# Performance work log

Measured on AMD Instinct MI355X. Metric: run time of the kernel, lower is better.

Reference implementation:

```python
import jax, jax.numpy as jnp
import numpy as np

N, E = 20000, 320000
IN, H, C = 1024, 8, 64
HC = H * C
EDGE_DIM = 16
NUM_GRAPHS = 8
LEAKY_SLOPE = 0.2
LN_EPS = 1e-5


def setup_inputs() -> dict:
    key = jax.random.key(0)
    ks = jax.random.split(key, 12)
    s = 0.05
    return {
        "x": jax.random.normal(ks[0], (N, IN), jnp.float32),
        "edge_attr": jax.random.normal(ks[1], (E, EDGE_DIM), jnp.float32),
        "edge_index": jax.random.randint(ks[2], (2, E), 0, N, dtype=jnp.int64),
        "batch": jnp.sort(jax.random.randint(ks[3], (N,), 0, NUM_GRAPHS, dtype=jnp.int64)),
        "W_src": jax.random.normal(ks[4], (IN, HC), jnp.float32) * s,
        "W_dst": jax.random.normal(ks[5], (IN, HC), jnp.float32) * s,
        "att_src": jax.random.normal(ks[6], (H, C), jnp.float32) * s,
        "att_dst": jax.random.normal(ks[7], (H, C), jnp.float32) * s,
        "bias": jnp.zeros((HC,), jnp.float32),
        "ln_gamma": jnp.ones((HC,), jnp.float32),
        "ln_beta": jnp.zeros((HC,), jnp.float32),
        "prelu_a": jnp.full((HC,), 0.25, jnp.float32),
    }


def reference(x, edge_attr, edge_index, batch, W_src, W_dst, att_src, att_dst,
              bias, ln_gamma, ln_beta, prelu_a):
    # Eval mode: node/edge feature dropout and attention dropout are identity.
    # with_edge == 'N': edge_attr is unused by the conv.
    n = x.shape[0]
    src, dst = edge_index[0], edge_index[1]

    xs = (x @ W_src).reshape(n, H, C)   # source-side projections
    xd = (x @ W_dst).reshape(n, H, C)   # dest-side projections
    a_src = jnp.einsum('nhc,hc->nh', xs, att_src)
    a_dst = jnp.einsum('nhc,hc->nh', xd, att_dst)

    # edge scores + softmax over incoming edges of each destination node
    e = jax.nn.leaky_relu(a_src[src] + a_dst[dst], LEAKY_SLOPE)  # [E,H]
    m = jax.ops.segment_max(e, dst, num_segments=n)              # [N,H]
    m = jax.lax.stop_gradient(jnp.where(jnp.isfinite(m), m, 0.0))
    ex = jnp.exp(e - m[dst])
    denom = jax.ops.segment_sum(ex, dst, num_segments=n)
    alpha = ex / (denom[dst] + 1e-16)                            # [E,H]

    msg = alpha[:, :, None] * xs[src]                            # [E,H,C]
    out = jax.ops.segment_sum(msg, dst, num_segments=n).reshape(n, HC) + bias

    # norm_type == 'layer': the per-graph boolean-mask loop applies LayerNorm
    # row-wise; with sorted batch ids this equals a single LayerNorm over all
    # nodes (LayerNorm has no cross-row statistics).
    mu = jnp.mean(out, axis=-1, keepdims=True)
    var = jnp.mean(jnp.square(out - mu), axis=-1, keepdims=True)
    y = (out - mu) * jax.lax.rsqrt(var + LN_EPS) * ln_gamma + ln_beta

    # PReLU with per-channel slope
    return jnp.where(y >= 0, y, prelu_a * y)
```

## Files before the change

### kernel.cpp

```cpp
#include <hip/hip_runtime.h>
#include <hip/hip_bf16.h>

#define N_NODES 20000
#define N_EDGES 320000
#define IN_DIM  1024
#define H_HEADS 8
#define C_CH    64
#define HC      512
#define LEAKY   0.2f
#define LN_EPS  1e-5f

#define BCOLS 576

typedef short bf16x8 __attribute__((ext_vector_type(8)));
typedef float f32x4  __attribute__((ext_vector_type(4)));

__device__ __forceinline__ unsigned short f2bf(float f) {
    union { float f; unsigned int u; } c; c.f = f;
    unsigned int u = c.u;
    unsigned int r = (u + 0x7fffu + ((u >> 16) & 1u)) >> 16;
    return (unsigned short)r;
}
__device__ __forceinline__ float bf2f(unsigned int h) {
    union { unsigned int u; float f; } c; c.u = h << 16; return c.f;
}
__device__ __forceinline__ void gload_lds16(const void* g, void* l) {
    __builtin_amdgcn_global_load_lds(
        (const __attribute__((address_space(1))) unsigned int*)g,
        (__attribute__((address_space(3))) unsigned int*)l, 16, 0, 0);
}

#define DEG_BLOCKS 1250
#define CONV_BLOCKS 2048

__global__ __launch_bounds__(256) void fused_pre(
        const float* __restrict__ x, short* __restrict__ xb,
        const int* __restrict__ ei, int* __restrict__ deg) {
    int t = threadIdx.x;
    if (blockIdx.x < DEG_BLOCKS) {
        int e = blockIdx.x * 256 + t;
        atomicAdd(&deg[ei[N_EDGES + e]], 1);
        return;
    }
    int bid = blockIdx.x - DEG_BLOCKS;
    const int total = N_NODES * IN_DIM / 8;
    int stride = CONV_BLOCKS * 256;
    for (int i = bid * 256 + t; i < total; i += stride) {
        float4 a = ((const float4*)x)[(size_t)i * 2];
        float4 b = ((const float4*)x)[(size_t)i * 2 + 1];
        uint4 r;
        r.x = (unsigned int)f2bf(a.x) | ((unsigned int)f2bf(a.y) << 16);
        r.y = (unsigned int)f2bf(a.z) | ((unsigned int)f2bf(a.w) << 16);
        r.z = (unsigned int)f2bf(b.x) | ((unsigned int)f2bf(b.y) << 16);
        r.w = (unsigned int)f2bf(b.z) | ((unsigned int)f2bf(b.w) << 16);
        *(uint4*)(&xb[(size_t)i * 8]) = r;
    }
}

__global__ void prep_w_scan(const float* __restrict__ Wsrc,
                            const float* __restrict__ Wdst,
                            const float* __restrict__ att_src,
                            const float* __restrict__ att_dst,
                            short* __restrict__ wbT,
                            const int* __restrict__ deg,
                            int* __restrict__ off,
                            int* __restrict__ cursor) {
    int t = threadIdx.x;

    if (blockIdx.x == IN_DIM) {
        __shared__ int wtot[2];
        int lane = t & 63, w = t >> 6;
        const int4* deg4 = (const int4*)deg;
        int s = 0;
        if (t < 125) {
            #pragma unroll
            for (int j = 0; j < 40; ++j) {
                int4 u = deg4[t * 40 + j];
                s += u.x + u.y + u.z + u.w;
            }
        }
        int v = s;
        #pragma unroll
        for (int o = 1; o < 64; o <<= 1) {
            int u = __shfl_up(v, o);
            if (lane >= o) v += u;
        }
        if (lane == 63) wtot[w] = v;
        __syncthreads();
        int add = (w == 1) ? wtot[0] : 0;
        int run = add + v - s;
        if (t < 125) {
            int4* off4 = (int4*)off;
            int4* cur4 = (int4*)cursor;
            #pragma unroll
            for (int j = 0; j < 40; ++j) {
                int4 u = deg4[t * 40 + j];
                int4 o_;
                o_.x = run;
                o_.y = o_.x + u.x;
                o_.z = o_.y + u.y;
                o_.w = o_.z + u.z;
                off4[t * 40 + j] = o_;
                cur4[t * 40 + j] = o_;
                run = o_.w + u.w;
            }
            if (t == 124) off[N_NODES] = run;
        }
        return;
    }

    int k = blockIdx.x;
    float4 v = *(const float4*)(Wsrc + (size_t)k * HC + t * 4);
    wbT[(size_t)(t * 4 + 0) * IN_DIM + k] = (short)f2bf(v.x);
    wbT[(size_t)(t * 4 + 1) * IN_DIM + k] = (short)f2bf(v.y);
    wbT[(size_t)(t * 4 + 2) * IN_DIM + k] = (short)f2bf(v.z);
    wbT[(size_t)(t * 4 + 3) * IN_DIM + k] = (short)f2bf(v.w);
    if (t < 16) {
        int h = t & 7;
        const float* W   = (t < 8) ? Wsrc : Wdst;
        const float* att = (t < 8) ? att_src : att_dst;
        float s = 0.f;
        #pragma unroll
        for (int c = 0; c < C_CH; ++c)
            s += W[(size_t)k * HC + h * C_CH + c] * att[h * C_CH + c];
        wbT[(size_t)(512 + t) * IN_DIM + k] = (short)f2bf(s);
    } else if (t < 64) {
        wbT[(size_t)(512 + t) * IN_DIM + k] = 0;
    }
}

#define BM 64
#define BN 96
#define BK 64
#define NCOLT (BCOLS / BN)
#define NROWT ((N_NODES + BM - 1) / BM)
#define NWG (NCOLT * NROWT)
#define KSTEPS (IN_DIM / BK)
#define A_SLOTS (BM * BK / 8)
#define B_SLOTS (BN * BK / 8)

__global__ __launch_bounds__(256) void gemm_scatter(
        const short* __restrict__ xb,
        const short* __restrict__ wbT,
        short* __restrict__ xsb,
        float* __restrict__ a_srcv,
        float* __restrict__ a_dstv,
        const int* __restrict__ ei,
        int* __restrict__ cursor,
        int* __restrict__ csr_src) {
    __shared__ short As[A_SLOTS * 8];
    __shared__ short Bs[B_SLOTS * 8];

    int t = threadIdx.x;

    if (blockIdx.x >= NWG) {
        int e = (blockIdx.x - NWG) * 256 + t;
        int d = ei[N_EDGES + e];
        int idx = atomicAdd(&cursor[d], 1);
        csr_src[idx] = ei[e];
        return;
    }

    int orig = blockIdx.x;
    const int q = NWG >> 3, r = NWG & 7;
    int xcd  = orig & 7;
    int wgid = (xcd < r ? xcd * (q + 1) : r * (q + 1) + (xcd - r) * q) + (orig >> 3);
    int col0 = (wgid % NCOLT) * BN;
    int row0 = (wgid / NCOLT) * BM;

    int lane = t & 63;
    int w    = t >> 6;
    int lr   = lane & 15;
    int lg   = lane >> 4;
    int sw   = lr & 7;
    int wr   = (w >> 1) * 32;
    int wc   = (w & 1) * 48;

    const short* a_base[2];
    #pragma unroll
    for (int i = 0; i < 2; ++i) {
        int s  = t + 256 * i;
        int m  = s >> 3;
        int kc = (s & 7) ^ (m & 7);
        int gm = row0 + m;
        if (gm >= N_NODES) gm = N_NODES - 1;
        a_base[i] = xb + (size_t)gm * IN_DIM + kc * 8;
    }
    const short* b_base[3];
    #pragma unroll
    for (int i = 0; i < 3; ++i) {
        int s  = t + 256 * i;
        int c  = s >> 3;
        int kc = (s & 7) ^ (c & 7);
        b_base[i] = wbT + (size_t)(col0 + c) * IN_DIM + kc * 8;
    }

    f32x4 acc[2][3] = {};

    for (int step = 0; step < KSTEPS; ++step) {
        int k0 = step * BK;
        #pragma unroll
        for (int i = 0; i < 2; ++i)
            gload_lds16(a_base[i] + k0, &As[(t + 256 * i) * 8]);
        #pragma unroll
        for (int i = 0; i < 3; ++i)
            gload_lds16(b_base[i] + k0, &Bs[(t + 256 * i) * 8]);
        asm volatile("s_waitcnt vmcnt(0)" ::: "memory");
        __builtin_amdgcn_s_barrier();

        #pragma unroll
        for (int ks = 0; ks < 2; ++ks) {
            int kc  = ks * 4 + lg;
            int kca = kc ^ sw;
            bf16x8 af[2], bfr[3];
            #pragma unroll
            for (int mi = 0; mi < 2; ++mi)
                af[mi] = *(const bf16x8*)(&As[((wr + mi * 16 + lr) * 8 + kca) * 8]);
            #pragma unroll
            for (int ni = 0; ni < 3; ++ni)
                bfr[ni] = *(const bf16x8*)(&Bs[((wc + ni * 16 + lr) * 8 + kca) * 8]);
            __builtin_amdgcn_s_setprio(1);
            #pragma unroll
            for (int mi = 0; mi < 2; ++mi)
                #pragma unroll
                for (int ni = 0; ni < 3; ++ni)
                    acc[mi][ni] = __builtin_amdgcn_mfma_f32_16x16x32_bf16(
                        af[mi], bfr[ni], acc[mi][ni], 0, 0, 0);
            __builtin_amdgcn_s_setprio(0);
        }
        __builtin_amdgcn_s_barrier();
    }

    #pragma unroll
    for (int mi = 0; mi < 2; ++mi) {
        #pragma unroll
        for (int rr = 0; rr < 4; ++rr) {
            int row = row0 + wr + mi * 16 + lg * 4 + rr;
            if (row >= N_NODES) continue;
            #pragma unroll
            for (int ni = 0; ni < 3; ++ni) {
                int col = col0 + wc + ni * 16 + lr;
                float v = acc[mi][ni][rr];
                if (col < 512)      xsb[(size_t)row * HC + col] = (short)f2bf(v);
                else if (col < 520) a_srcv[(size_t)row * 8 + (col - 512)] = v;
                else if (col < 528) a_dstv[(size_t)row * 8 + (col - 520)] = v;
            }
        }
    }
}

__global__ __launch_bounds__(256) void aggregate_ln(
        const int* __restrict__ off,
        const int* __restrict__ csr_src,
        const float* __restrict__ a_srcv,
        const float* __restrict__ a_dstv,
        const short* __restrict__ xsb,
        const float* __restrict__ bias,
        const float* __restrict__ gamma,
        const float* __restrict__ beta,
        const float* __restrict__ prelu_a,
        float* __restrict__ out) {
    int lane = threadIdx.x & 63;
    int n    = blockIdx.x * 4 + (threadIdx.x >> 6);
    int ch0  = lane * 8;
    int h    = lane >> 3;

    int start = off[n], end = off[n + 1];
    float ad  = a_dstv[(size_t)n * 8 + h];

    float acc[8] = {};
    float wsum = 0.f;

    int i = start;
    for (; i + 1 < end; i += 2) {
        int s0 = __builtin_amdgcn_readfirstlane(csr_src[i]);
        int s1 = __builtin_amdgcn_readfirstlane(csr_src[i + 1]);
        float sc0 = a_srcv[(size_t)s0 * 8 + h] + ad;
        float sc1 = a_srcv[(size_t)s1 * 8 + h] + ad;
        uint4 u0 = *(const uint4*)(xsb + (size_t)s0 * HC + ch0);
        uint4 u1 = *(const uint4*)(xsb + (size_t)s1 * HC + ch0);
        sc0 = (sc0 >= 0.f) ? sc0 : LEAKY * sc0;
        sc1 = (sc1 >= 0.f) ? sc1 : LEAKY * sc1;
        float w0 = __expf(sc0);
        float w1 = __expf(sc1);
        acc[0] = fmaf(w0, bf2f(u0.x & 0xffffu), acc[0]);
        acc[1] = fmaf(w0, bf2f(u0.x >> 16),     acc[1]);
        acc[2] = fmaf(w0, bf2f(u0.y & 0xffffu), acc[2]);
        acc[3] = fmaf(w0, bf2f(u0.y >> 16),     acc[3]);
        acc[4] = fmaf(w0, bf2f(u0.z & 0xffffu), acc[4]);
        acc[5] = fmaf(w0, bf2f(u0.z >> 16),     acc[5]);
        acc[6] = fmaf(w0, bf2f(u0.w & 0xffffu), acc[6]);
        acc[7] = fmaf(w0, bf2f(u0.w >> 16),     acc[7]);
        acc[0] = fmaf(w1, bf2f(u1.x & 0xffffu), acc[0]);
        acc[1] = fmaf(w1, bf2f(u1.x >> 16),     acc[1]);
        acc[2] = fmaf(w1, bf2f(u1.y & 0xffffu), acc[2]);
        acc[3] = fmaf(w1, bf2f(u1.y >> 16),     acc[3]);
        acc[4] = fmaf(w1, bf2f(u1.z & 0xffffu), acc[4]);
        acc[5] = fmaf(w1, bf2f(u1.z >> 16),     acc[5]);
        acc[6] = fmaf(w1, bf2f(u1.w & 0xffffu), acc[6]);
        acc[7] = fmaf(w1, bf2f(u1.w >> 16),     acc[7]);
        wsum += w0 + w1;
    }
    if (i < end) {
        int s0 = __builtin_amdgcn_readfirstlane(csr_src[i]);
        float sc0 = a_srcv[(size_t)s0 * 8 + h] + ad;
        uint4 u0 = *(const uint4*)(xsb + (size_t)s0 * HC + ch0);
        sc0 = (sc0 >= 0.f) ? sc0 : LEAKY * sc0;
        float w0 = __expf(sc0);
        acc[0] = fmaf(w0, bf2f(u0.x & 0xffffu), acc[0]);
        acc[1] = fmaf(w0, bf2f(u0.x >> 16),     acc[1]);
        acc[2] = fmaf(w0, bf2f(u0.y & 0xffffu), acc[2]);
        acc[3] = fmaf(w0, bf2f(u0.y >> 16),     acc[3]);
        acc[4] = fmaf(w0, bf2f(u0.z & 0xffffu), acc[4]);
        acc[5] = fmaf(w0, bf2f(u0.z >> 16),     acc[5]);
        acc[6] = fmaf(w0, bf2f(u0.w & 0xffffu), acc[6]);
        acc[7] = fmaf(w0, bf2f(u0.w >> 16),     acc[7]);
        wsum += w0;
    }

    float inv = 1.f / (wsum + 1e-16f);
    float4 b0 = *(const float4*)(bias + ch0);
    float4 b1 = *(const float4*)(bias + ch0 + 4);
    float v8[8];
    float psum = 0.f, psq = 0.f;
    const float bb[8] = {b0.x, b0.y, b0.z, b0.w, b1.x, b1.y, b1.z, b1.w};
    #pragma unroll
    for (int j = 0; j < 8; ++j) {
        v8[j] = acc[j] * inv + bb[j];
        psum += v8[j];
        psq  += v8[j] * v8[j];
    }
    #pragma unroll
    for (int o = 32; o > 0; o >>= 1) {
        psum += __shfl_xor(psum, o);
        psq  += __shfl_xor(psq, o);
    }
    float mu   = psum * (1.f / (float)HC);
    float var  = psq * (1.f / (float)HC) - mu * mu;
    float rstd = rsqrtf(var + LN_EPS);

    float4 g0 = *(const float4*)(gamma + ch0);
    float4 g1 = *(const float4*)(gamma + ch0 + 4);
    float4 e0 = *(const float4*)(beta + ch0);
    float4 e1 = *(const float4*)(beta + ch0 + 4);
    float4 p0 = *(const float4*)(prelu_a + ch0);
    float4 p1 = *(const float4*)(prelu_a + ch0 + 4);
    const float gg[8] = {g0.x, g0.y, g0.z, g0.w, g1.x, g1.y, g1.z, g1.w};
    const float ee[8] = {e0.x, e0.y, e0.z, e0.w, e1.x, e1.y, e1.z, e1.w};
    const float pp[8] = {p0.x, p0.y, p0.z, p0.w, p1.x, p1.y, p1.z, p1.w};
    float y[8];
    #pragma unroll
    for (int j = 0; j < 8; ++j) {
        float v = (v8[j] - mu) * rstd * gg[j] + ee[j];
        y[j] = (v >= 0.f) ? v : pp[j] * v;
    }
    float4* o4 = (float4*)(out + (size_t)n * HC + ch0);
    o4[0] = make_float4(y[0], y[1], y[2], y[3]);
    o4[1] = make_float4(y[4], y[5], y[6], y[7]);
}

extern "C" void kernel_launch(void* const* d_in, const int* in_sizes, int n_in,
                              void* d_out, int out_size, void* d_ws, size_t ws_size,
                              hipStream_t stream) {
    const float* x        = (const float*)d_in[0];
    const int*   ei       = (const int*)d_in[2];
    const float* Wsrc     = (const float*)d_in[4];
    const float* Wdst     = (const float*)d_in[5];
    const float* att_src  = (const float*)d_in[6];
    const float* att_dst  = (const float*)d_in[7];
    const float* bias     = (const float*)d_in[8];
    const float* gamma    = (const float*)d_in[9];
    const float* beta     = (const float*)d_in[10];
    const float* prelu_a  = (const float*)d_in[11];
    float* out            = (float*)d_out;

    char*  ws = (char*)d_ws;
    size_t o  = 0;
    auto alloc = [&](size_t bytes) -> void* {
        void* p = ws + o;
        o += (bytes + 255) & ~(size_t)255;
        return p;
    };
    short* wbT     = (short*)alloc(sizeof(short) * BCOLS * IN_DIM);
    short* xsb     = (short*)alloc(sizeof(short) * (size_t)N_NODES * HC);
    float* a_srcv  = (float*)alloc(sizeof(float) * N_NODES * 8);
    float* a_dstv  = (float*)alloc(sizeof(float) * N_NODES * 8);
    int*   deg     = (int*)alloc(sizeof(int) * N_NODES);
    int*   off     = (int*)alloc(sizeof(int) * (N_NODES + 1));
    int*   cursor  = (int*)alloc(sizeof(int) * N_NODES);
    int*   csr_src = (int*)alloc(sizeof(int) * N_EDGES);

    short* xb = (short*)d_out;

    hipMemsetAsync(deg, 0, sizeof(int) * N_NODES, stream);

    fused_pre<<<DEG_BLOCKS + CONV_BLOCKS, 256, 0, stream>>>(x, xb, ei, deg);

    prep_w_scan<<<IN_DIM + 1, 128, 0, stream>>>(Wsrc, Wdst, att_src, att_dst,
                                                wbT, deg, off, cursor);

    gemm_scatter<<<NWG + DEG_BLOCKS, 256, 0, stream>>>(
        xb, wbT, xsb, a_srcv, a_dstv, ei, cursor, csr_src);

    aggregate_ln<<<N_NODES / 4, 256, 0, stream>>>(
        off, csr_src, a_srcv, a_dstv, xsb, bias, gamma, beta, prelu_a, out);
}
```

Baseline: 154.7 us.

## Fuse fp32-to-bf16 conversion of x into GEMM A-tile loading

Removes the separate pass that converted x to a bf16 scratch buffer. The GEMM now reads fp32 x directly, converts it in registers, and stores the bf16 A tile to LDS, while B still uses async global-to-LDS loads. This saves a full write and re-read of the bf16 copy. In exchange, each x row is read as fp32 by all six column tiles instead of as bf16, and A loads become synchronous register round-trips without prefetch overlap.

```diff
diff --git a/kernel.cpp b/kernel.cpp
--- a/kernel.cpp
+++ b/kernel.cpp
@@ -24,6 +24,9 @@
 __device__ __forceinline__ float bf2f(unsigned int h) {
     union { unsigned int u; float f; } c; c.u = h << 16; return c.f;
 }
+__device__ __forceinline__ unsigned int bfpack(float lo, float hi) {
+    return (unsigned int)f2bf(lo) | ((unsigned int)f2bf(hi) << 16);
+}
 __device__ __forceinline__ void gload_lds16(const void* g, void* l) {
     __builtin_amdgcn_global_load_lds(
         (const __attribute__((address_space(1))) unsigned int*)g,
@@ -31,30 +34,11 @@
 }
 
 #define DEG_BLOCKS 1250
-#define CONV_BLOCKS 2048
-
-__global__ __launch_bounds__(256) void fused_pre(
-        const float* __restrict__ x, short* __restrict__ xb,
+
+__global__ __launch_bounds__(256) void deg_hist(
         const int* __restrict__ ei, int* __restrict__ deg) {
-    int t = threadIdx.x;
-    if (blockIdx.x < DEG_BLOCKS) {
-        int e = blockIdx.x * 256 + t;
-        atomicAdd(&deg[ei[N_EDGES + e]], 1);
-        return;
-    }
-    int bid = blockIdx.x - DEG_BLOCKS;
-    const int total = N_NODES * IN_DIM / 8;
-    int stride = CONV_BLOCKS * 256;
-    for (int i = bid * 256 + t; i < total; i += stride) {
-        float4 a = ((const float4*)x)[(size_t)i * 2];
-        float4 b = ((const float4*)x)[(size_t)i * 2 + 1];
-        uint4 r;
-        r.x = (unsigned int)f2bf(a.x) | ((unsigned int)f2bf(a.y) << 16);
-        r.y = (unsigned int)f2bf(a.z) | ((unsigned int)f2bf(a.w) << 16);
-        r.z = (unsigned int)f2bf(b.x) | ((unsigned int)f2bf(b.y) << 16);
-        r.w = (unsigned int)f2bf(b.z) | ((unsigned int)f2bf(b.w) << 16);
-        *(uint4*)(&xb[(size_t)i * 8]) = r;
-    }
+    int e = blockIdx.x * 256 + threadIdx.x;
+    atomicAdd(&deg[ei[N_EDGES + e]], 1);
 }
 
 __global__ void prep_w_scan(const float* __restrict__ Wsrc,
@@ -140,7 +124,7 @@
 #define B_SLOTS (BN * BK / 8)
 
 __global__ __launch_bounds__(256) void gemm_scatter(
-        const short* __restrict__ xb,
+        const float* __restrict__ x,
         const short* __restrict__ wbT,
         short* __restrict__ xsb,
         float* __restrict__ a_srcv,
@@ -176,7 +160,7 @@
     int wr   = (w >> 1) * 32;
     int wc   = (w & 1) * 48;
 
-    const short* a_base[2];
+    const float* a_base[2];
     #pragma unroll
     for (int i = 0; i < 2; ++i) {
         int s  = t + 256 * i;
@@ -184,7 +168,7 @@
         int kc = (s & 7) ^ (m & 7);
         int gm = row0 + m;
         if (gm >= N_NODES) gm = N_NODES - 1;
-        a_base[i] = xb + (size_t)gm * IN_DIM + kc * 8;
+        a_base[i] = x + (size_t)gm * IN_DIM + kc * 8;
     }
     const short* b_base[3];
     #pragma unroll
@@ -200,13 +184,20 @@
     for (int step = 0; step < KSTEPS; ++step) {
         int k0 = step * BK;
         #pragma unroll
-        for (int i = 0; i < 2; ++i)
-            gload_lds16(a_base[i] + k0, &As[(t + 256 * i) * 8]);
+        for (int i = 0; i < 2; ++i) {
+            float4 fa = *(const float4*)(a_base[i] + k0);
+            float4 fb = *(const float4*)(a_base[i] + k0 + 4);
+            uint4 rr;
+            rr.x = bfpack(fa.x, fa.y);
+            rr.y = bfpack(fa.z, fa.w);
+            rr.z = bfpack(fb.x, fb.y);
+            rr.w = bfpack(fb.z, fb.w);
+            *(uint4*)(&As[(t + 256 * i) * 8]) = rr;
+        }
         #pragma unroll
         for (int i = 0; i < 3; ++i)
             gload_lds16(b_base[i] + k0, &Bs[(t + 256 * i) * 8]);
-        asm volatile("s_waitcnt vmcnt(0)" ::: "memory");
-        __builtin_amdgcn_s_barrier();
+        __syncthreads();
 
         #pragma unroll
         for (int ks = 0; ks < 2; ++ks) {
@@ -228,7 +219,7 @@
                         af[mi], bfr[ni], acc[mi][ni], 0, 0, 0);
             __builtin_amdgcn_s_setprio(0);
         }
-        __builtin_amdgcn_s_barrier();
+        __syncthreads();
     }
 
     #pragma unroll
@@ -390,17 +381,15 @@
     int*   cursor  = (int*)alloc(sizeof(int) * N_NODES);
     int*   csr_src = (int*)alloc(sizeof(int) * N_EDGES);
 
-    short* xb = (short*)d_out;
-
     hipMemsetAsync(deg, 0, sizeof(int) * N_NODES, stream);
 
-    fused_pre<<<DEG_BLOCKS + CONV_BLOCKS, 256, 0, stream>>>(x, xb, ei, deg);
+    deg_hist<<<DEG_BLOCKS, 256, 0, stream>>>(ei, deg);
 
     prep_w_scan<<<IN_DIM + 1, 128, 0, stream>>>(Wsrc, Wdst, att_src, att_dst,
                                                 wbT, deg, off, cursor);
 
     gemm_scatter<<<NWG + DEG_BLOCKS, 256, 0, stream>>>(
-        xb, wbT, xsb, a_srcv, a_dstv, ei, cursor, csr_src);
+        x, wbT, xsb, a_srcv, a_dstv, ei, cursor, csr_src);
 
     aggregate_ln<<<N_NODES / 4, 256, 0, stream>>>(
         off, csr_src, a_srcv, a_dstv, xsb, bias, gamma, beta, prelu_a, out);
```

Result: faster. 148.0 us (-4.4%).

## Regroup pre-pass kernels and unroll edge aggregation loop by four

Applied to the files above, without the earlier changes.

The degree histogram becomes its own kernel, and the x-to-bf16 conversion is fused with the weight transpose and prefix scan into one mid-pass kernel. The weight prep now overlaps with the large conversion instead of running in a separate launch. The aggregation loop is unrolled to four edges per iteration through a macro, so more gathers can be in flight per wave. In exchange, the weight-prep and scan blocks run at 256 threads with half of them idle, and the unroll adds register pressure.

```diff
diff --git a/kernel.cpp b/kernel.cpp
--- a/kernel.cpp
+++ b/kernel.cpp
@@ -31,101 +31,103 @@
 }
 
 #define DEG_BLOCKS 1250
+
+__global__ __launch_bounds__(256) void deg_hist(
+        const int* __restrict__ ei, int* __restrict__ deg) {
+    int e = blockIdx.x * 256 + threadIdx.x;
+    atomicAdd(&deg[ei[N_EDGES + e]], 1);
+}
+
 #define CONV_BLOCKS 2048
-
-__global__ __launch_bounds__(256) void fused_pre(
+#define PREP_BLOCKS 1024
+
+__global__ __launch_bounds__(256) void mid_pass(
         const float* __restrict__ x, short* __restrict__ xb,
-        const int* __restrict__ ei, int* __restrict__ deg) {
-    int t = threadIdx.x;
-    if (blockIdx.x < DEG_BLOCKS) {
-        int e = blockIdx.x * 256 + t;
-        atomicAdd(&deg[ei[N_EDGES + e]], 1);
+        const float* __restrict__ Wsrc, const float* __restrict__ Wdst,
+        const float* __restrict__ att_src, const float* __restrict__ att_dst,
+        short* __restrict__ wbT,
+        const int* __restrict__ deg, int* __restrict__ off,
+        int* __restrict__ cursor) {
+    int t   = threadIdx.x;
+    int bid = blockIdx.x;
+
+    if (bid < CONV_BLOCKS) {
+        const int total = N_NODES * IN_DIM / 8;
+        int stride = CONV_BLOCKS * 256;
+        for (int i = bid * 256 + t; i < total; i += stride) {
+            float4 a = ((const float4*)x)[(size_t)i * 2];
+            float4 b = ((const float4*)x)[(size_t)i * 2 + 1];
+            uint4 r;
+            r.x = (unsigned int)f2bf(a.x) | ((unsigned int)f2bf(a.y) << 16);
+            r.y = (unsigned int)f2bf(a.z) | ((unsigned int)f2bf(a.w) << 16);
+            r.z = (unsigned int)f2bf(b.x) | ((unsigned int)f2bf(b.y) << 16);
+            r.w = (unsigned int)f2bf(b.z) | ((unsigned int)f2bf(b.w) << 16);
+            *(uint4*)(&xb[(size_t)i * 8]) = r;
+        }
         return;
     }
-    int bid = blockIdx.x - DEG_BLOCKS;
-    const int total = N_NODES * IN_DIM / 8;
-    int stride = CONV_BLOCKS * 256;
-    for (int i = bid * 256 + t; i < total; i += stride) {
-        float4 a = ((const float4*)x)[(size_t)i * 2];
-        float4 b = ((const float4*)x)[(size_t)i * 2 + 1];
-        uint4 r;
-        r.x = (unsigned int)f2bf(a.x) | ((unsigned int)f2bf(a.y) << 16);
-        r.y = (unsigned int)f2bf(a.z) | ((unsigned int)f2bf(a.w) << 16);
-        r.z = (unsigned int)f2bf(b.x) | ((unsigned int)f2bf(b.y) << 16);
-        r.w = (unsigned int)f2bf(b.z) | ((unsigned int)f2bf(b.w) << 16);
-        *(uint4*)(&xb[(size_t)i * 8]) = r;
-    }
-}
-
-__global__ void prep_w_scan(const float* __restrict__ Wsrc,
-                            const float* __restrict__ Wdst,
-                            const float* __restrict__ att_src,
-                            const float* __restrict__ att_dst,
-                            short* __restrict__ wbT,
-                            const int* __restrict__ deg,
-                            int* __restrict__ off,
-                            int* __restrict__ cursor) {
-    int t = threadIdx.x;
-
-    if (blockIdx.x == IN_DIM) {
-        __shared__ int wtot[2];
-        int lane = t & 63, w = t >> 6;
-        const int4* deg4 = (const int4*)deg;
-        int s = 0;
-        if (t < 125) {
-            #pragma unroll
-            for (int j = 0; j < 40; ++j) {
-                int4 u = deg4[t * 40 + j];
-                s += u.x + u.y + u.z + u.w;
-            }
-        }
-        int v = s;
-        #pragma unroll
-        for (int o = 1; o < 64; o <<= 1) {
-            int u = __shfl_up(v, o);
-            if (lane >= o) v += u;
-        }
-        if (lane == 63) wtot[w] = v;
-        __syncthreads();
-        int add = (w == 1) ? wtot[0] : 0;
-        int run = add + v - s;
-        if (t < 125) {
-            int4* off4 = (int4*)off;
-            int4* cur4 = (int4*)cursor;
-            #pragma unroll
-            for (int j = 0; j < 40; ++j) {
-                int4 u = deg4[t * 40 + j];
-                int4 o_;
-                o_.x = run;
-                o_.y = o_.x + u.x;
-                o_.z = o_.y + u.y;
-                o_.w = o_.z + u.z;
-                off4[t * 40 + j] = o_;
-                cur4[t * 40 + j] = o_;
-                run = o_.w + u.w;
-            }
-            if (t == 124) off[N_NODES] = run;
+
+    if (bid < CONV_BLOCKS + PREP_BLOCKS) {
+        if (t >= 128) return;
+        int k = bid - CONV_BLOCKS;
+        float4 v = *(const float4*)(Wsrc + (size_t)k * HC + t * 4);
+        wbT[(size_t)(t * 4 + 0) * IN_DIM + k] = (short)f2bf(v.x);
+        wbT[(size_t)(t * 4 + 1) * IN_DIM + k] = (short)f2bf(v.y);
+        wbT[(size_t)(t * 4 + 2) * IN_DIM + k] = (short)f2bf(v.z);
+        wbT[(size_t)(t * 4 + 3) * IN_DIM + k] = (short)f2bf(v.w);
+        if (t < 16) {
+            int h = t & 7;
+            const float* W   = (t < 8) ? Wsrc : Wdst;
+            const float* att = (t < 8) ? att_src : att_dst;
+            float s = 0.f;
+            #pragma unroll
+            for (int c = 0; c < C_CH; ++c)
+                s += W[(size_t)k * HC + h * C_CH + c] * att[h * C_CH + c];
+            wbT[(size_t)(512 + t) * IN_DIM + k] = (short)f2bf(s);
+        } else if (t < 64) {
+            wbT[(size_t)(512 + t) * IN_DIM + k] = 0;
         }
         return;
     }
 
-    int k = blockIdx.x;
-    float4 v = *(const float4*)(Wsrc + (size_t)k * HC + t * 4);
-    wbT[(size_t)(t * 4 + 0) * IN_DIM + k] = (short)f2bf(v.x);
-    wbT[(size_t)(t * 4 + 1) * IN_DIM + k] = (short)f2bf(v.y);
-    wbT[(size_t)(t * 4 + 2) * IN_DIM + k] = (short)f2bf(v.z);
-    wbT[(size_t)(t * 4 + 3) * IN_DIM + k] = (short)f2bf(v.w);
-    if (t < 16) {
-        int h = t & 7;
-        const float* W   = (t < 8) ? Wsrc : Wdst;
-        const float* att = (t < 8) ? att_src : att_dst;
-        float s = 0.f;
-        #pragma unroll
-        for (int c = 0; c < C_CH; ++c)
-            s += W[(size_t)k * HC + h * C_CH + c] * att[h * C_CH + c];
-        wbT[(size_t)(512 + t) * IN_DIM + k] = (short)f2bf(s);
-    } else if (t < 64) {
-        wbT[(size_t)(512 + t) * IN_DIM + k] = 0;
+    if (t >= 128) return;
+    __shared__ int wtot[2];
+    int lane = t & 63, w = t >> 6;
+    const int4* deg4 = (const int4*)deg;
+    int s = 0;
+    if (t < 125) {
+        #pragma unroll
+        for (int j = 0; j < 40; ++j) {
+            int4 u = deg4[t * 40 + j];
+            s += u.x + u.y + u.z + u.w;
+        }
+    }
+    int v = s;
+    #pragma unroll
+    for (int o = 1; o < 64; o <<= 1) {
+        int u = __shfl_up(v, o);
+        if (lane >= o) v += u;
+    }
+    if (lane == 63) wtot[w] = v;
+    __syncthreads();
+    int add = (w == 1) ? wtot[0] : 0;
+    int run = add + v - s;
+    if (t < 125) {
+        int4* off4 = (int4*)off;
+        int4* cur4 = (int4*)cursor;
+        #pragma unroll
+        for (int j = 0; j < 40; ++j) {
+            int4 u = deg4[t * 40 + j];
+            int4 o_;
+            o_.x = run;
+            o_.y = o_.x + u.x;
+            o_.z = o_.y + u.y;
+            o_.w = o_.z + u.z;
+            off4[t * 40 + j] = o_;
+            cur4[t * 40 + j] = o_;
+            run = o_.w + u.w;
+        }
+        if (t == 124) off[N_NODES] = run;
     }
 }
 
@@ -271,52 +273,36 @@
     float acc[8] = {};
     float wsum = 0.f;
 
+#define EDGE_ACC(sv)                                                          \
+    do {                                                                      \
+        float sc_ = a_srcv[(size_t)(sv) * 8 + h] + ad;                        \
+        uint4 u_  = *(const uint4*)(xsb + (size_t)(sv) * HC + ch0);           \
+        sc_ = (sc_ >= 0.f) ? sc_ : LEAKY * sc_;                               \
+        float w_ = __expf(sc_);                                               \
+        acc[0] = fmaf(w_, bf2f(u_.x & 0xffffu), acc[0]);                      \
+        acc[1] = fmaf(w_, bf2f(u_.x >> 16),     acc[1]);                      \
+        acc[2] = fmaf(w_, bf2f(u_.y & 0xffffu), acc[2]);                      \
+        acc[3] = fmaf(w_, bf2f(u_.y >> 16),     acc[3]);                      \
+        acc[4] = fmaf(w_, bf2f(u_.z & 0xffffu), acc[4]);                      \
+        acc[5] = fmaf(w_, bf2f(u_.z >> 16),     acc[5]);                      \
+        acc[6] = fmaf(w_, bf2f(u_.w & 0xffffu), acc[6]);                      \
+        acc[7] = fmaf(w_, bf2f(u_.w >> 16),     acc[7]);                      \
+        wsum += w_;                                                           \
+    } while (0)
+
     int i = start;
-    for (; i + 1 < end; i += 2) {
+    for (; i + 3 < end; i += 4) {
         int s0 = __builtin_amdgcn_readfirstlane(csr_src[i]);
         int s1 = __builtin_amdgcn_readfirstlane(csr_src[i + 1]);
-        float sc0 = a_srcv[(size_t)s0 * 8 + h] + ad;
-        float sc1 = a_srcv[(size_t)s1 * 8 + h] + ad;
-        uint4 u0 = *(const uint4*)(xsb + (size_t)s0 * HC + ch0);
-        uint4 u1 = *(const uint4*)(xsb + (size_t)s1 * HC + ch0);
-        sc0 = (sc0 >= 0.f) ? sc0 : LEAKY * sc0;
-        sc1 = (sc1 >= 0.f) ? sc1 : LEAKY * sc1;
-        float w0 = __expf(sc0);
-        float w1 = __expf(sc1);
-        acc[0] = fmaf(w0, bf2f(u0.x & 0xffffu), acc[0]);
-        acc[1] = fmaf(w0, bf2f(u0.x >> 16),     acc[1]);
-        acc[2] = fmaf(w0, bf2f(u0.y & 0xffffu), acc[2]);
-        acc[3] = fmaf(w0, bf2f(u0.y >> 16),     acc[3]);
-        acc[4] = fmaf(w0, bf2f(u0.z & 0xffffu), acc[4]);
-        acc[5] = fmaf(w0, bf2f(u0.z >> 16),     acc[5]);
-        acc[6] = fmaf(w0, bf2f(u0.w & 0xffffu), acc[6]);
-        acc[7] = fmaf(w0, bf2f(u0.w >> 16),     acc[7]);
-        acc[0] = fmaf(w1, bf2f(u1.x & 0xffffu), acc[0]);
-        acc[1] = fmaf(w1, bf2f(u1.x >> 16),     acc[1]);
-        acc[2] = fmaf(w1, bf2f(u1.y & 0xffffu), acc[2]);
-        acc[3] = fmaf(w1, bf2f(u1.y >> 16),     acc[3]);
-        acc[4] = fmaf(w1, bf2f(u1.z & 0xffffu), acc[4]);
-        acc[5] = fmaf(w1, bf2f(u1.z >> 16),     acc[5]);
-        acc[6] = fmaf(w1, bf2f(u1.w & 0xffffu), acc[6]);
-        acc[7] = fmaf(w1, bf2f(u1.w >> 16),     acc[7]);
-        wsum += w0 + w1;
-    }
-    if (i < end) {
+        int s2 = __builtin_amdgcn_readfirstlane(csr_src[i + 2]);
+        int s3 = __builtin_amdgcn_readfirstlane(csr_src[i + 3]);
+        EDGE_ACC(s0); EDGE_ACC(s1); EDGE_ACC(s2); EDGE_ACC(s3);
+    }
+    for (; i < end; ++i) {
         int s0 = __builtin_amdgcn_readfirstlane(csr_src[i]);
-        float sc0 = a_srcv[(size_t)s0 * 8 + h] + ad;
-        uint4 u0 = *(const uint4*)(xsb + (size_t)s0 * HC + ch0);
-        sc0 = (sc0 >= 0.f) ? sc0 : LEAKY * sc0;
-        float w0 = __expf(sc0);
-        acc[0] = fmaf(w0, bf2f(u0.x & 0xffffu), acc[0]);
-        acc[1] = fmaf(w0, bf2f(u0.x >> 16),     acc[1]);
-        acc[2] = fmaf(w0, bf2f(u0.y & 0xffffu), acc[2]);
-        acc[3] = fmaf(w0, bf2f(u0.y >> 16),     acc[3]);
-        acc[4] = fmaf(w0, bf2f(u0.z & 0xffffu), acc[4]);
-        acc[5] = fmaf(w0, bf2f(u0.z >> 16),     acc[5]);
-        acc[6] = fmaf(w0, bf2f(u0.w & 0xffffu), acc[6]);
-        acc[7] = fmaf(w0, bf2f(u0.w >> 16),     acc[7]);
-        wsum += w0;
-    }
+        EDGE_ACC(s0);
+    }
+#undef EDGE_ACC
 
     float inv = 1.f / (wsum + 1e-16f);
     float4 b0 = *(const float4*)(bias + ch0);
@@ -394,10 +380,10 @@
 
     hipMemsetAsync(deg, 0, sizeof(int) * N_NODES, stream);
 
-    fused_pre<<<DEG_BLOCKS + CONV_BLOCKS, 256, 0, stream>>>(x, xb, ei, deg);
-
-    prep_w_scan<<<IN_DIM + 1, 128, 0, stream>>>(Wsrc, Wdst, att_src, att_dst,
-                                                wbT, deg, off, cursor);
+    deg_hist<<<DEG_BLOCKS, 256, 0, stream>>>(ei, deg);
+
+    mid_pass<<<CONV_BLOCKS + PREP_BLOCKS + 1, 256, 0, stream>>>(
+        x, xb, Wsrc, Wdst, att_src, att_dst, wbT, deg, off, cursor);
 
     gemm_scatter<<<NWG + DEG_BLOCKS, 256, 0, stream>>>(
         xb, wbT, xsb, a_srcv, a_dstv, ei, cursor, csr_src);
```

After: 152.9 us. No clear change (-1.2%).
